# Kernel optimization log

Measured on AMD Instinct MI355X. Metric: run time of the kernel, lower is better.

Reference implementation:

```python
import jax, jax.numpy as jnp
import numpy as np

KS = 8        # hardcoded kernel size in MWPT
FIL_LEN = 8   # chosen filter length (db4-style), so pad pl = 0


def _transform_matrix():
    # mat[row, idx] = (-1)**idx for idx = KS-1 .. 0, scaled by (-1)**(FIL_LEN//2)
    mat = np.zeros((KS, KS), dtype=np.float32)
    for row, idx in enumerate(range(KS - 1, -1, -1)):
        mat[row, idx] = (-1.0) ** idx
    mat *= (-1.0) ** (FIL_LEN // 2)
    return jnp.asarray(mat)


def setup_inputs() -> dict:
    key = jax.random.key(0)
    k1, k2 = jax.random.split(key)
    x = jax.random.normal(k1, (128, 1, 65536), dtype=jnp.float32)
    kernel = jax.random.normal(k2, (1, 1, KS), dtype=jnp.float32)
    return {"x": x, "kernel": kernel}


def _conv(x, w):
    # circular pad (ks//2-1, ks//2-1) then stride-2 cross-correlation, halves T
    xp = jnp.pad(x, ((0, 0), (0, 0), (KS // 2 - 1, KS // 2 - 1)), mode='wrap')
    return jax.lax.conv_general_dilated(
        xp, w, window_strides=(2,), padding='VALID',
        dimension_numbers=('NCH', 'OIH', 'NCH'))


def _fwd(x, kernel):
    mat = _transform_matrix()
    k_lo = kernel                                   # low-pass
    k_hi = jnp.einsum('oik,kj->oij', kernel, mat)   # kernel @ mat, high-pass QMF
    # level 1: node 0 -> (0 low, 4 high)
    a0 = _conv(x, k_lo)
    a4 = _conv(x, k_hi)
    # level 2: 0->(0,2), 4->(4,6)
    b0 = _conv(a0, k_lo); b2 = _conv(a0, k_hi)
    b4 = _conv(a4, k_lo); b6 = _conv(a4, k_hi)
    # level 3: 0->(0,1), 2->(2,3), 4->(4,5), 6->(6,7)
    c0 = _conv(b0, k_lo); c1 = _conv(b0, k_hi)
    c2 = _conv(b2, k_lo); c3 = _conv(b2, k_hi)
    c4 = _conv(b4, k_lo); c5 = _conv(b4, k_hi)
    c6 = _conv(b6, k_lo); c7 = _conv(b6, k_hi)
    # forward() compacts each level's list then reindexes with gray code i^(i>>1)
    level1 = jnp.stack([a0, a4], axis=2)                       # [B,1,2,T/2]
    level2 = jnp.stack([b0, b2, b6, b4], axis=2)               # gray of [b0,b2,b4,b6]
    level3 = jnp.stack([c0, c1, c3, c2, c6, c7, c5, c4], axis=2)  # gray of c0..c7
    return level1, level2, level3


def reference(x, kernel):
    return _fwd(x, kernel)
```

## Files before the change

### kernel.cpp

```cpp
#include <hip/hip_runtime.h>


#define T_LEN   65536
#define T_MASK  65535
#define HALO_L  21
#define CHUNK   2048
#define LOAD_N  (CHUNK + 48)
#define PADIDX(i) ((i) + ((i) >> 3))

__global__ __launch_bounds__(256) void mwpt_kernel(
    const float* __restrict__ x, const float* __restrict__ ker,
    float* __restrict__ out)
{
    __shared__ float xl[PADIDX(LOAD_N - 1) + 1];

    const int t   = threadIdx.x;
    const int seg = blockIdx.x;
    const int bi  = blockIdx.y;
    const int base = seg * CHUNK;
    const float* __restrict__ xrow = x + (size_t)bi * T_LEN;

    for (int i = t; i < LOAD_N; i += 256) {
        int g = (base + i - HALO_L) & T_MASK;
        xl[PADIDX(i)] = xrow[g];
    }

    float lo[8], hi[8];
#pragma unroll
    for (int j = 0; j < 8; ++j) lo[j] = ker[j];
#pragma unroll
    for (int j = 0; j < 8; ++j) hi[j] = (j & 1) ? -ker[7 - j] : ker[7 - j];

    __syncthreads();

    float xw[50];
    const int wbase = 9 * t;
#pragma unroll
    for (int j = 0; j < 50; ++j) xw[j] = xl[wbase + j + (j >> 3)];

    float a0v[22], a4v[22];
#pragma unroll
    for (int i = 0; i < 22; ++i) {
        float s0 = 0.f, s4 = 0.f;
#pragma unroll
        for (int k = 0; k < 8; ++k) {
            float xv = xw[2 * i + k];
            s0 += xv * lo[k];
            s4 += xv * hi[k];
        }
        a0v[i] = s0; a4v[i] = s4;
    }

    float b0v[8], b2v[8], b4v[8], b6v[8];
#pragma unroll
    for (int j = 0; j < 8; ++j) {
        float s0 = 0.f, s2 = 0.f, s4 = 0.f, s6 = 0.f;
#pragma unroll
        for (int k = 0; k < 8; ++k) {
            float v0 = a0v[2 * j + k], v4 = a4v[2 * j + k];
            s0 += v0 * lo[k]; s2 += v0 * hi[k];
            s4 += v4 * lo[k]; s6 += v4 * hi[k];
        }
        b0v[j] = s0; b2v[j] = s2; b4v[j] = s4; b6v[j] = s6;
    }

    float c[8] = {0, 0, 0, 0, 0, 0, 0, 0};
#pragma unroll
    for (int k = 0; k < 8; ++k) {
        c[0] += b0v[k] * lo[k]; c[1] += b0v[k] * hi[k];
        c[2] += b2v[k] * lo[k]; c[3] += b2v[k] * hi[k];
        c[4] += b4v[k] * lo[k]; c[5] += b4v[k] * hi[k];
        c[6] += b6v[k] * lo[k]; c[7] += b6v[k] * hi[k];
    }

    const int n3 = seg * 256 + t;

    {
        size_t o = (size_t)bi * 65536 + 4 * (size_t)n3;
        *(float4*)(out + o)         = make_float4(a0v[9], a0v[10], a0v[11], a0v[12]);
        *(float4*)(out + o + 32768) = make_float4(a4v[9], a4v[10], a4v[11], a4v[12]);
    }
    {
        size_t o = 8388608ull + (size_t)bi * 65536 + 2 * (size_t)n3;
        *(float2*)(out + o)             = make_float2(b0v[3], b0v[4]);
        *(float2*)(out + o + 16384)     = make_float2(b2v[3], b2v[4]);
        *(float2*)(out + o + 2 * 16384) = make_float2(b6v[3], b6v[4]);
        *(float2*)(out + o + 3 * 16384) = make_float2(b4v[3], b4v[4]);
    }
    {
        size_t o = 16777216ull + (size_t)bi * 65536 + (size_t)n3;
        out[o]            = c[0];
        out[o + 8192]     = c[1];
        out[o + 2 * 8192] = c[3];
        out[o + 3 * 8192] = c[2];
        out[o + 4 * 8192] = c[6];
        out[o + 5 * 8192] = c[7];
        out[o + 6 * 8192] = c[5];
        out[o + 7 * 8192] = c[4];
    }
}

extern "C" void kernel_launch(void* const* d_in, const int* in_sizes, int n_in,
                              void* d_out, int out_size, void* d_ws, size_t ws_size,
                              hipStream_t stream) {
    const float* x   = (const float*)d_in[0];
    const float* ker = (const float*)d_in[1];
    float* out = (float*)d_out;
    dim3 grid(32, 128), block(256);
    hipLaunchKernelGGL(mwpt_kernel, grid, block, 0, stream, x, ker, out);
}
```

Measured before the change: 146.5 us.

## Stage intermediate wavelet levels through LDS to remove redundant halo recomputation

Instead of each thread recomputing a 22-wide level-1 window and 8-wide level-2 window from registers (heavy overlap between threads), each level is now computed once per block, stored in shared memory, and read back by the next level after a barrier. A few edge threads compute the halo elements. This cuts redundant FMAs and register pressure (xw[50], a0v[22], etc.) at the cost of two extra __syncthreads and more LDS traffic and space.

```diff
diff --git a/kernel.cpp b/kernel.cpp
--- a/kernel.cpp
+++ b/kernel.cpp
@@ -1,102 +1,158 @@
 #include <hip/hip_runtime.h>
 
 
-#define T_LEN   65536
 #define T_MASK  65535
-#define HALO_L  21
-#define CHUNK   2048
-#define LOAD_N  (CHUNK + 48)
-#define PADIDX(i) ((i) + ((i) >> 3))
+#define PAD(i)  ((i) + ((i) >> 3))
+
+#define XS_N 2090
+#define AS_N 1042
+#define BS_N 518
+#define XS_P (PAD(XS_N - 1) + 1)
+#define AS_P (PAD(AS_N - 1) + 1)
+#define BS_P (PAD(BS_N - 1) + 1)
 
 __global__ __launch_bounds__(256) void mwpt_kernel(
     const float* __restrict__ x, const float* __restrict__ ker,
     float* __restrict__ out)
 {
-    __shared__ float xl[PADIDX(LOAD_N - 1) + 1];
+    __shared__ float lds[XS_P + 2 * AS_P];
+    float* xs  = lds;
+    float* as0 = lds + XS_P;
+    float* as1 = lds + XS_P + AS_P;
+    float* bs0 = lds;
+    float* bs1 = lds + BS_P;
+    float* bs2 = lds + 2 * BS_P;
+    float* bs3 = lds + 3 * BS_P;
 
     const int t   = threadIdx.x;
     const int seg = blockIdx.x;
     const int bi  = blockIdx.y;
-    const int base = seg * CHUNK;
-    const float* __restrict__ xrow = x + (size_t)bi * T_LEN;
+    const int N3  = seg * 256;
+    const int N2  = seg * 512;
+    const int N1  = seg * 1024;
+    const float* __restrict__ xrow = x + (size_t)bi * 65536;
 
-    for (int i = t; i < LOAD_N; i += 256) {
-        int g = (base + i - HALO_L) & T_MASK;
-        xl[PADIDX(i)] = xrow[g];
-    }
+    const int xg0 = 2 * N1 - 21;
+    for (int i = t; i < XS_N; i += 256)
+        xs[PAD(i)] = xrow[(xg0 + i) & T_MASK];
 
     float lo[8], hi[8];
 #pragma unroll
-    for (int j = 0; j < 8; ++j) lo[j] = ker[j];
+    for (int k = 0; k < 8; ++k) lo[k] = ker[k];
 #pragma unroll
-    for (int j = 0; j < 8; ++j) hi[j] = (j & 1) ? -ker[7 - j] : ker[7 - j];
+    for (int k = 0; k < 8; ++k) hi[k] = (k & 1) ? -ker[7 - k] : ker[7 - k];
 
     __syncthreads();
 
-    float xw[50];
-    const int wbase = 9 * t;
+    {
+        const int j0 = 4 * t + 9;
+        float xv[14];
 #pragma unroll
-    for (int j = 0; j < 50; ++j) xw[j] = xl[wbase + j + (j >> 3)];
+        for (int q = 0; q < 14; ++q) xv[q] = xs[PAD(2 * j0 + q)];
+        float r0[4], r4[4];
+#pragma unroll
+        for (int i = 0; i < 4; ++i) {
+            float s0 = 0.f, s4 = 0.f;
+#pragma unroll
+            for (int k = 0; k < 8; ++k) {
+                float v = xv[2 * i + k];
+                s0 += v * lo[k]; s4 += v * hi[k];
+            }
+            r0[i] = s0; r4[i] = s4;
+        }
+#pragma unroll
+        for (int i = 0; i < 4; ++i) {
+            as0[PAD(j0 + i)] = r0[i];
+            as1[PAD(j0 + i)] = r4[i];
+        }
+        if (t < 18) {
+            int j = (t < 9) ? t : (1024 + t);
+            float s0 = 0.f, s4 = 0.f;
+#pragma unroll
+            for (int k = 0; k < 8; ++k) {
+                float v = xs[PAD(2 * j + k)];
+                s0 += v * lo[k]; s4 += v * hi[k];
+            }
+            as0[PAD(j)] = s0; as1[PAD(j)] = s4;
+        }
+        size_t o = (size_t)bi * 65536 + (size_t)N1 + 4 * (size_t)t;
+        *(float4*)(out + o)         = make_float4(r0[0], r0[1], r0[2], r0[3]);
+        *(float4*)(out + o + 32768) = make_float4(r4[0], r4[1], r4[2], r4[3]);
+    }
 
-    float a0v[22], a4v[22];
+    __syncthreads();
+
+    {
+        const int m0 = 2 * t + 3;
+        float av0[10], av1[10];
 #pragma unroll
-    for (int i = 0; i < 22; ++i) {
-        float s0 = 0.f, s4 = 0.f;
+        for (int q = 0; q < 10; ++q) {
+            av0[q] = as0[PAD(2 * m0 + q)];
+            av1[q] = as1[PAD(2 * m0 + q)];
+        }
+        float v0[2], v2[2], v4[2], v6[2];
+#pragma unroll
+        for (int j = 0; j < 2; ++j) {
+            float s0 = 0.f, s2 = 0.f, s4 = 0.f, s6 = 0.f;
+#pragma unroll
+            for (int k = 0; k < 8; ++k) {
+                float a0 = av0[2 * j + k], a4 = av1[2 * j + k];
+                s0 += a0 * lo[k]; s2 += a0 * hi[k];
+                s4 += a4 * lo[k]; s6 += a4 * hi[k];
+            }
+            v0[j] = s0; v2[j] = s2; v4[j] = s4; v6[j] = s6;
+        }
+#pragma unroll
+        for (int j = 0; j < 2; ++j) {
+            bs0[PAD(m0 + j)] = v0[j];
+            bs1[PAD(m0 + j)] = v2[j];
+            bs2[PAD(m0 + j)] = v4[j];
+            bs3[PAD(m0 + j)] = v6[j];
+        }
+        if (t < 6) {
+            int m = (t < 3) ? t : (512 + t);
+            float s0 = 0.f, s2 = 0.f, s4 = 0.f, s6 = 0.f;
+#pragma unroll
+            for (int k = 0; k < 8; ++k) {
+                float a0 = as0[PAD(2 * m + k)], a4 = as1[PAD(2 * m + k)];
+                s0 += a0 * lo[k]; s2 += a0 * hi[k];
+                s4 += a4 * lo[k]; s6 += a4 * hi[k];
+            }
+            bs0[PAD(m)] = s0; bs1[PAD(m)] = s2;
+            bs2[PAD(m)] = s4; bs3[PAD(m)] = s6;
+        }
+        size_t o = 8388608ull + (size_t)bi * 65536 + (size_t)N2 + 2 * (size_t)t;
+        *(float2*)(out + o)             = make_float2(v0[0], v0[1]);
+        *(float2*)(out + o + 16384)     = make_float2(v2[0], v2[1]);
+        *(float2*)(out + o + 2 * 16384) = make_float2(v6[0], v6[1]);
+        *(float2*)(out + o + 3 * 16384) = make_float2(v4[0], v4[1]);
+    }
+
+    __syncthreads();
+
+    {
+        float c0 = 0.f, c1 = 0.f, c2 = 0.f, c3 = 0.f;
+        float c4 = 0.f, c5 = 0.f, c6 = 0.f, c7 = 0.f;
 #pragma unroll
         for (int k = 0; k < 8; ++k) {
-            float xv = xw[2 * i + k];
-            s0 += xv * lo[k];
-            s4 += xv * hi[k];
+            float b0 = bs0[PAD(2 * t + k)];
+            float b2 = bs1[PAD(2 * t + k)];
+            float b4 = bs2[PAD(2 * t + k)];
+            float b6 = bs3[PAD(2 * t + k)];
+            c0 += b0 * lo[k]; c1 += b0 * hi[k];
+            c2 += b2 * lo[k]; c3 += b2 * hi[k];
+            c4 += b4 * lo[k]; c5 += b4 * hi[k];
+            c6 += b6 * lo[k]; c7 += b6 * hi[k];
         }
-        a0v[i] = s0; a4v[i] = s4;
-    }
-
-    float b0v[8], b2v[8], b4v[8], b6v[8];
-#pragma unroll
-    for (int j = 0; j < 8; ++j) {
-        float s0 = 0.f, s2 = 0.f, s4 = 0.f, s6 = 0.f;
-#pragma unroll
-        for (int k = 0; k < 8; ++k) {
-            float v0 = a0v[2 * j + k], v4 = a4v[2 * j + k];
-            s0 += v0 * lo[k]; s2 += v0 * hi[k];
-            s4 += v4 * lo[k]; s6 += v4 * hi[k];
-        }
-        b0v[j] = s0; b2v[j] = s2; b4v[j] = s4; b6v[j] = s6;
-    }
-
-    float c[8] = {0, 0, 0, 0, 0, 0, 0, 0};
-#pragma unroll
-    for (int k = 0; k < 8; ++k) {
-        c[0] += b0v[k] * lo[k]; c[1] += b0v[k] * hi[k];
-        c[2] += b2v[k] * lo[k]; c[3] += b2v[k] * hi[k];
-        c[4] += b4v[k] * lo[k]; c[5] += b4v[k] * hi[k];
-        c[6] += b6v[k] * lo[k]; c[7] += b6v[k] * hi[k];
-    }
-
-    const int n3 = seg * 256 + t;
-
-    {
-        size_t o = (size_t)bi * 65536 + 4 * (size_t)n3;
-        *(float4*)(out + o)         = make_float4(a0v[9], a0v[10], a0v[11], a0v[12]);
-        *(float4*)(out + o + 32768) = make_float4(a4v[9], a4v[10], a4v[11], a4v[12]);
-    }
-    {
-        size_t o = 8388608ull + (size_t)bi * 65536 + 2 * (size_t)n3;
-        *(float2*)(out + o)             = make_float2(b0v[3], b0v[4]);
-        *(float2*)(out + o + 16384)     = make_float2(b2v[3], b2v[4]);
-        *(float2*)(out + o + 2 * 16384) = make_float2(b6v[3], b6v[4]);
-        *(float2*)(out + o + 3 * 16384) = make_float2(b4v[3], b4v[4]);
-    }
-    {
-        size_t o = 16777216ull + (size_t)bi * 65536 + (size_t)n3;
-        out[o]            = c[0];
-        out[o + 8192]     = c[1];
-        out[o + 2 * 8192] = c[3];
-        out[o + 3 * 8192] = c[2];
-        out[o + 4 * 8192] = c[6];
-        out[o + 5 * 8192] = c[7];
-        out[o + 6 * 8192] = c[5];
-        out[o + 7 * 8192] = c[4];
+        size_t o = 16777216ull + (size_t)bi * 65536 + (size_t)N3 + (size_t)t;
+        out[o]            = c0;
+        out[o + 8192]     = c1;
+        out[o + 2 * 8192] = c3;
+        out[o + 3 * 8192] = c2;
+        out[o + 4 * 8192] = c6;
+        out[o + 5 * 8192] = c7;
+        out[o + 6 * 8192] = c5;
+        out[o + 7 * 8192] = c4;
     }
 }
 
```

After: 131.0 us. 1.12x faster.
